# Optimization experiments

Hardware: AMD Instinct MI355X
Metric: run time of the kernel (lower is better)

Reference implementation:

```python
import jax, jax.numpy as jnp
import numpy as np

BN_EPS = 1e-5

def _bn(x, p):
    # p rows: gamma, beta, running_mean, running_var (eval-mode BatchNorm1d)
    g, b, m, v = p[0], p[1], p[2], p[3]
    return (x - m) * jax.lax.rsqrt(v + BN_EPS) * g + b

def setup_inputs() -> dict:
    key = jax.random.key(0)
    ks = iter(jax.random.split(key, 32))
    B, P, T, E, H = 16, 64, 8, 64, 64
    batch = B * P
    def w(shape, scale=0.1):
        return (jax.random.normal(next(ks), shape, dtype=jnp.float32) * scale)
    def bn_pack(d):
        k1, k2, k3, k4 = jax.random.split(next(ks), 4)
        gamma = 1.0 + 0.1 * jax.random.normal(k1, (d,), dtype=jnp.float32)
        beta = 0.1 * jax.random.normal(k2, (d,), dtype=jnp.float32)
        mean = 0.1 * jax.random.normal(k3, (d,), dtype=jnp.float32)
        var = 0.5 + jax.random.uniform(k4, (d,), dtype=jnp.float32)
        return jnp.stack([gamma, beta, mean, var], axis=0)
    return {
        "h_states": w((1, batch, H), 1.0),
        "end_pos": w((batch, 2), 1.0),
        "vx": w((T, batch), 1.0),
        "vy": w((T, batch), 1.0),
        "agent_type": jax.random.uniform(next(ks), (T, batch, 1), dtype=jnp.float32),
        "ws_w": w((2, E)), "ws_b": w((E,)),
        "wv_w": w((2, E)), "wv_b": w((E,)),
        "wa_w": w((6, E)), "wa_b": w((E,)),
        "att1_w": w((E, 1024)), "att1_b": w((1024,)), "att_bn1": bn_pack(1024),
        "att2_w": w((1024, 1)), "att2_b": w((1,)), "att_bn2": bn_pack(1),
        "pre1_w": w((E + H, 512)), "pre1_b": w((512,)), "pre_bn1": bn_pack(512),
        "pre2_w": w((512, 1024)), "pre2_b": w((1024,)), "pre_bn2": bn_pack(1024),
        "num_ped": P,
    }

def reference(h_states, end_pos, vx, vy, agent_type,
              ws_w, ws_b, wv_w, wv_b, wa_w, wa_b,
              att1_w, att1_b, att_bn1, att2_w, att2_b, att_bn2,
              pre1_w, pre1_b, pre_bn1, pre2_w, pre2_b, pre_bn2,
              num_ped):
    P = num_ped
    batch = end_pos.shape[0]
    B = batch // P  # uniform groups (seq_start_end = [(b*P, (b+1)*P)])
    H = h_states.shape[-1]
    h = h_states.reshape(batch, H).reshape(B, P, H)            # curr_hidden per group
    pos = end_pos.reshape(B, P, 2)
    # k = i*P + j: repeated row = pos[j], 'transposed' row = pos[i]
    rel = pos[:, None, :, :] - pos[:, :, None, :]               # [B, i, j, 2]
    rel_emb = rel @ ws_w + ws_b                                 # [B, i, j, E]
    # attention_mlp: Linear->BN->ReLU->Linear->BN->ReLU (make_mlp applies BN+act after every layer)
    a1 = jax.nn.relu(_bn(rel_emb @ att1_w + att1_b, att_bn1))   # [B, i, j, 1024]
    scores = jax.nn.relu(_bn(a1 @ att2_w + att2_b, att_bn2))    # [B, i, j, 1]
    # torch.softmax(scores, dim=1) on shape (n*n, 1): softmax over a singleton -> all ones
    aw = jax.nn.softmax(scores, axis=-1)
    # velocity embedding: computed in the original then discarded (dead code, kept for fidelity)
    vel = jnp.stack([vx[-1].reshape(B, P), vy[-1].reshape(B, P)], axis=-1)
    _vel_emb = vel @ wv_w + wv_b  # noqa: F841 (unused, matches original)
    # curr_agent_type.repeat(num_ped, 6): row k=i*P+j -> type[j] tiled to 6 features
    at6 = jnp.repeat(agent_type[0].reshape(B, P, 1), 6, axis=-1)  # [B, j, 6]
    at_emb = at6 @ wa_w + wa_b                                    # [B, j, E]
    feat_j = jnp.concatenate([h, at_emb], axis=-1)                # [B, j, H+E]
    weighted = jnp.broadcast_to(feat_j[:, None, :, :], (B, P, P, feat_j.shape[-1])) * (0.05 * aw)
    p1 = jax.nn.relu(_bn(weighted @ pre1_w + pre1_b, pre_bn1))    # [B, i, j, 512]
    p2 = jax.nn.relu(_bn(p1 @ pre2_w + pre2_b, pre_bn2))          # [B, i, j, 1024]
    pool = p2.max(axis=2)                                         # view(n,n,-1).max(1): max over j
    return pool.reshape(batch, -1)
```

## Files before the change

### kernel.cpp

```cpp
#include <hip/hip_runtime.h>
#include <hip/hip_bf16.h>

#define BN_EPS 1e-5f

typedef float f32x4 __attribute__((ext_vector_type(4)));
typedef __bf16 bfx8 __attribute__((ext_vector_type(8)));


__global__ __launch_bounds__(256) void k0_prep(
    const float* __restrict__ w2, const float* __restrict__ w1,
    __bf16* __restrict__ w2t, __bf16* __restrict__ w1t)
{
    __shared__ float tile[64][69];
    const int t = threadIdx.x;
    int kt0, n0, src_ld, dst_ld;
    const float* src;
    __bf16* dst;
    if (blockIdx.x < 128) {
        kt0 = (blockIdx.x & 7) * 64;  n0 = (blockIdx.x >> 3) * 64;
        src = w2; src_ld = 1024; dst = w2t; dst_ld = 512;
    } else {
        const int bt = blockIdx.x - 128;
        kt0 = (bt & 1) * 64;  n0 = (bt >> 1) * 64;
        src = w1; src_ld = 512; dst = w1t; dst_ld = 128;
    }
    #pragma unroll
    for (int i = 0; i < 4; ++i) {
        const int idx = t + i * 256;
        const int kk  = idx >> 4;
        const int nq  = (idx & 15) * 4;
        const f32x4 val = *(const f32x4*)&src[(size_t)(kt0 + kk) * src_ld + n0 + nq];
        #pragma unroll
        for (int j = 0; j < 4; ++j) tile[kk][nq + j] = val[j];
    }
    __syncthreads();
    #pragma unroll
    for (int i = 0; i < 2; ++i) {
        const int idx = t + i * 256;
        const int n   = idx >> 3;
        const int kq  = (idx & 7) * 8;
        bfx8 o;
        #pragma unroll
        for (int j = 0; j < 8; ++j) o[j] = (__bf16)tile[kq + j][n];
        *(bfx8*)&dst[(size_t)(n0 + n) * dst_ld + kt0 + kq] = o;
    }
}

__global__ __launch_bounds__(512, 2) void kmain(
    const float* __restrict__ h,
    const float* __restrict__ at,
    const float* __restrict__ wa_w,
    const float* __restrict__ wa_b,
    const __bf16* __restrict__ w1t,
    const float* __restrict__ b1,
    const float* __restrict__ bn1,
    const __bf16* __restrict__ w2t,
    const float* __restrict__ b2,
    const float* __restrict__ bn2,
    float* __restrict__ out)
{
    const int cc   = blockIdx.x;
    const int b    = blockIdx.y;
    const int t    = threadIdx.x;
    const int wid  = t >> 6;
    const int lane = t & 63;
    const int l15  = lane & 15;
    const int lhi  = lane >> 4;

    __shared__ __bf16 x_lds[64][136];
    __shared__ __bf16 p1_lds[64][520];
    __shared__ __bf16 B2_lds[64][520];
    __shared__ float  red[4][64];

    f32x4 b2stage[8];
    {
        const char* base = (const char*)w2t + (size_t)(cc * 64) * 1024;
        #pragma unroll
        for (int i = 0; i < 8; ++i) {
            const int n = i * 8 + wid;
            b2stage[i] = *(const f32x4*)(base + (size_t)n * 1024 + lane * 16);
        }
    }

    if (t < 64) {
        float s = 0.f;
        #pragma unroll
        for (int q = 0; q < 6; ++q) s += wa_w[q * 64 + t];
        red[0][t] = s;
    }
    __syncthreads();

    #pragma unroll
    for (int i = 0; i < 2; ++i) {
        const int idx = t + i * 512;
        const int rr  = idx >> 4;
        const int cg  = (idx & 15) * 8;
        bfx8 o;
        if (cg < 64) {
            const f32x4 v0 = *(const f32x4*)&h[(size_t)(b * 64 + rr) * 64 + cg];
            const f32x4 v1 = *(const f32x4*)&h[(size_t)(b * 64 + rr) * 64 + cg + 4];
            #pragma unroll
            for (int j = 0; j < 4; ++j) {
                o[j]     = (__bf16)(0.05f * v0[j]);
                o[4 + j] = (__bf16)(0.05f * v1[j]);
            }
        } else {
            const float a = at[b * 64 + rr];
            #pragma unroll
            for (int j = 0; j < 8; ++j) {
                const int e = cg - 64 + j;
                o[j] = (__bf16)(0.05f * fmaf(a, red[0][e], wa_b[e]));
            }
        }
        *(bfx8*)&x_lds[rr][cg] = o;
    }
    __syncthreads();

    const int n0w = wid * 64;
    bfx8 b1r[16];
    #pragma unroll
    for (int ks = 0; ks < 4; ++ks)
        #pragma unroll
        for (int nf = 0; nf < 4; ++nf)
            b1r[ks * 4 + nf] = *(const bfx8*)(w1t +
                (size_t)(n0w + nf * 16 + l15) * 128 + ks * 32 + lhi * 8);

    f32x4 acc1[4][4] = {};
    #pragma unroll
    for (int ks = 0; ks < 4; ++ks) {
        bfx8 a[4];
        #pragma unroll
        for (int mf = 0; mf < 4; ++mf)
            a[mf] = *(const bfx8*)&x_lds[mf * 16 + l15][ks * 32 + lhi * 8];
        #pragma unroll
        for (int mf = 0; mf < 4; ++mf)
            #pragma unroll
            for (int nf = 0; nf < 4; ++nf)
                acc1[mf][nf] = __builtin_amdgcn_mfma_f32_16x16x32_bf16(
                    a[mf], b1r[ks * 4 + nf], acc1[mf][nf], 0, 0, 0);
    }

    #pragma unroll
    for (int nf = 0; nf < 4; ++nf) {
        const int c    = n0w + nf * 16 + l15;
        const float s  = rsqrtf(bn1[1536 + c] + BN_EPS) * bn1[c];
        const float be = bn1[512 + c];
        const float mu = bn1[1024 + c];
        const float bias = b1[c];
        #pragma unroll
        for (int mf = 0; mf < 4; ++mf)
            #pragma unroll
            for (int r = 0; r < 4; ++r) {
                const float val =
                    fmaxf((acc1[mf][nf][r] + bias - mu) * s + be, 0.f);
                p1_lds[mf * 16 + lhi * 4 + r][c] = (__bf16)val;
            }
    }

    #pragma unroll
    for (int i = 0; i < 8; ++i) {
        const int n = i * 8 + wid;
        *(f32x4*)((char*)&B2_lds[0][0] + (size_t)n * 1040 + lane * 16) =
            b2stage[i];
    }
    __syncthreads();

    const int mw = wid >> 1;
    const int nw = wid & 1;
    f32x4 acc2[2] = {};
    #pragma unroll
    for (int ks = 0; ks < 16; ++ks) {
        const bfx8 a = *(const bfx8*)&p1_lds[mw * 16 + l15][ks * 32 + lhi * 8];
        #pragma unroll
        for (int f = 0; f < 2; ++f) {
            const bfx8 bb =
                *(const bfx8*)&B2_lds[nw * 32 + f * 16 + l15][ks * 32 + lhi * 8];
            acc2[f] = __builtin_amdgcn_mfma_f32_16x16x32_bf16(a, bb, acc2[f], 0, 0, 0);
        }
    }

    #pragma unroll
    for (int f = 0; f < 2; ++f) {
        const int cg   = cc * 64 + nw * 32 + f * 16 + l15;
        const float s  = rsqrtf(bn2[3072 + cg] + BN_EPS) * bn2[cg];
        const float be = bn2[1024 + cg];
        const float mu = bn2[2048 + cg];
        const float bias = b2[cg];
        float mm = 0.f;
        #pragma unroll
        for (int r = 0; r < 4; ++r) {
            const float val = (acc2[f][r] + bias - mu) * s + be;
            mm = fmaxf(mm, fmaxf(val, 0.f));
        }
        mm = fmaxf(mm, __shfl_xor(mm, 16));
        mm = fmaxf(mm, __shfl_xor(mm, 32));
        if (lane < 16) red[mw][nw * 32 + f * 16 + lane] = mm;
    }
    __syncthreads();

    const int cl   = t & 63;
    const int iseg = t >> 6;
    const float pool = fmaxf(fmaxf(red[0][cl], red[1][cl]),
                             fmaxf(red[2][cl], red[3][cl]));
    const int ob = (b * 64 + iseg * 8) * 1024 + cc * 64 + cl;
    #pragma unroll
    for (int ii = 0; ii < 8; ++ii) out[ob + ii * 1024] = pool;
}

extern "C" void kernel_launch(void* const* d_in, const int* in_sizes, int n_in,
                              void* d_out, int out_size, void* d_ws, size_t ws_size,
                              hipStream_t stream) {
    const float* h    = (const float*)d_in[0];
    const float* at   = (const float*)d_in[4];
    const float* wa_w = (const float*)d_in[9];
    const float* wa_b = (const float*)d_in[10];
    const float* w1   = (const float*)d_in[17];
    const float* b1   = (const float*)d_in[18];
    const float* bn1  = (const float*)d_in[19];
    const float* w2   = (const float*)d_in[20];
    const float* b2   = (const float*)d_in[21];
    const float* bn2  = (const float*)d_in[22];

    char* ws = (char*)d_ws;
    __bf16* w2t = (__bf16*)ws;
    __bf16* w1t = (__bf16*)(ws + (1 << 20));
    float*  out = (float*)d_out;

    k0_prep<<<144, 256, 0, stream>>>(w2, w1, w2t, w1t);
    kmain<<<dim3(16, 16), 512, 0, stream>>>(h, at, wa_w, wa_b,
                                            w1t, b1, bn1, w2t, b2, bn2, out);
}
```

Baseline: 21.06 us.

## Hoist activation prep and BN folding into prep kernel; vectorize LDS and output stores

```diff
diff --git a/kernel.cpp b/kernel.cpp
--- a/kernel.cpp
+++ b/kernel.cpp
@@ -5,58 +5,107 @@
 
 typedef float f32x4 __attribute__((ext_vector_type(4)));
 typedef __bf16 bfx8 __attribute__((ext_vector_type(8)));
+typedef __bf16 bfx4 __attribute__((ext_vector_type(4)));
 
 
 __global__ __launch_bounds__(256) void k0_prep(
     const float* __restrict__ w2, const float* __restrict__ w1,
-    __bf16* __restrict__ w2t, __bf16* __restrict__ w1t)
+    const float* __restrict__ h, const float* __restrict__ at,
+    const float* __restrict__ wa_w, const float* __restrict__ wa_b,
+    const float* __restrict__ b1, const float* __restrict__ bn1,
+    const float* __restrict__ b2, const float* __restrict__ bn2,
+    __bf16* __restrict__ w2t, __bf16* __restrict__ w1t,
+    __bf16* __restrict__ xg, float* __restrict__ scsh)
 {
-    __shared__ float tile[64][69];
-    const int t = threadIdx.x;
-    int kt0, n0, src_ld, dst_ld;
-    const float* src;
-    __bf16* dst;
-    if (blockIdx.x < 128) {
-        kt0 = (blockIdx.x & 7) * 64;  n0 = (blockIdx.x >> 3) * 64;
-        src = w2; src_ld = 1024; dst = w2t; dst_ld = 512;
+    const int t  = threadIdx.x;
+    const int bx = blockIdx.x;
+
+    if (bx < 144) {
+        __shared__ float tile[64][69];
+        int kt0, n0, src_ld, dst_ld;
+        const float* src;
+        __bf16* dst;
+        if (bx < 128) {
+            kt0 = (bx & 7) * 64;  n0 = (bx >> 3) * 64;
+            src = w2; src_ld = 1024; dst = w2t; dst_ld = 512;
+        } else {
+            const int bt = bx - 128;
+            kt0 = (bt & 1) * 64;  n0 = (bt >> 1) * 64;
+            src = w1; src_ld = 512; dst = w1t; dst_ld = 128;
+        }
+        #pragma unroll
+        for (int i = 0; i < 4; ++i) {
+            const int idx = t + i * 256;
+            const int kk  = idx >> 4;
+            const int nq  = (idx & 15) * 4;
+            const f32x4 val = *(const f32x4*)&src[(size_t)(kt0 + kk) * src_ld + n0 + nq];
+            #pragma unroll
+            for (int j = 0; j < 4; ++j) tile[kk][nq + j] = val[j];
+        }
+        __syncthreads();
+        #pragma unroll
+        for (int i = 0; i < 2; ++i) {
+            const int idx = t + i * 256;
+            const int n   = idx >> 3;
+            const int kq  = (idx & 7) * 8;
+            bfx8 o;
+            #pragma unroll
+            for (int j = 0; j < 8; ++j) o[j] = (__bf16)tile[kq + j][n];
+            *(bfx8*)&dst[(size_t)(n0 + n) * dst_ld + kt0 + kq] = o;
+        }
+    } else if (bx < 160) {
+        __shared__ float S[64];
+        const int r0 = (bx - 144) * 64;
+        if (t < 64) {
+            float s = 0.f;
+            #pragma unroll
+            for (int q = 0; q < 6; ++q) s += wa_w[q * 64 + t];
+            S[t] = s;
+        }
+        __syncthreads();
+        #pragma unroll
+        for (int i = 0; i < 4; ++i) {
+            const int idx = t + i * 256;
+            const int row = idx >> 4;
+            const int cg  = (idx & 15) * 8;
+            bfx8 o;
+            if (cg < 64) {
+                const f32x4 v0 = *(const f32x4*)&h[(size_t)(r0 + row) * 64 + cg];
+                const f32x4 v1 = *(const f32x4*)&h[(size_t)(r0 + row) * 64 + cg + 4];
+                #pragma unroll
+                for (int j = 0; j < 4; ++j) {
+                    o[j]     = (__bf16)(0.05f * v0[j]);
+                    o[4 + j] = (__bf16)(0.05f * v1[j]);
+                }
+            } else {
+                const float a = at[r0 + row];
+                #pragma unroll
+                for (int j = 0; j < 8; ++j) {
+                    const int e = cg - 64 + j;
+                    o[j] = (__bf16)(0.05f * fmaf(a, S[e], wa_b[e]));
+                }
+            }
+            *(bfx8*)&xg[(size_t)(r0 + row) * 128 + cg] = o;
+        }
     } else {
-        const int bt = blockIdx.x - 128;
-        kt0 = (bt & 1) * 64;  n0 = (bt >> 1) * 64;
-        src = w1; src_ld = 512; dst = w1t; dst_ld = 128;
-    }
-    #pragma unroll
-    for (int i = 0; i < 4; ++i) {
-        const int idx = t + i * 256;
-        const int kk  = idx >> 4;
-        const int nq  = (idx & 15) * 4;
-        const f32x4 val = *(const f32x4*)&src[(size_t)(kt0 + kk) * src_ld + n0 + nq];
-        #pragma unroll
-        for (int j = 0; j < 4; ++j) tile[kk][nq + j] = val[j];
-    }
-    __syncthreads();
-    #pragma unroll
-    for (int i = 0; i < 2; ++i) {
-        const int idx = t + i * 256;
-        const int n   = idx >> 3;
-        const int kq  = (idx & 7) * 8;
-        bfx8 o;
-        #pragma unroll
-        for (int j = 0; j < 8; ++j) o[j] = (__bf16)tile[kq + j][n];
-        *(bfx8*)&dst[(size_t)(n0 + n) * dst_ld + kt0 + kq] = o;
+        for (int c = t; c < 512; c += 256) {
+            const float s = rsqrtf(bn1[1536 + c] + BN_EPS) * bn1[c];
+            scsh[c]       = s;
+            scsh[512 + c] = (b1[c] - bn1[1024 + c]) * s + bn1[512 + c];
+        }
+        for (int c = t; c < 1024; c += 256) {
+            const float s  = rsqrtf(bn2[3072 + c] + BN_EPS) * bn2[c];
+            scsh[1024 + c] = s;
+            scsh[2048 + c] = (b2[c] - bn2[2048 + c]) * s + bn2[1024 + c];
+        }
     }
 }
 
 __global__ __launch_bounds__(512, 2) void kmain(
-    const float* __restrict__ h,
-    const float* __restrict__ at,
-    const float* __restrict__ wa_w,
-    const float* __restrict__ wa_b,
+    const __bf16* __restrict__ xg,
     const __bf16* __restrict__ w1t,
-    const float* __restrict__ b1,
-    const float* __restrict__ bn1,
     const __bf16* __restrict__ w2t,
-    const float* __restrict__ b2,
-    const float* __restrict__ bn2,
+    const float* __restrict__ scsh,
     float* __restrict__ out)
 {
     const int cc   = blockIdx.x;
@@ -74,86 +123,63 @@
 
     f32x4 b2stage[8];
     {
-        const char* base = (const char*)w2t + (size_t)(cc * 64) * 1024;
+        const __bf16* base = w2t + (size_t)(cc * 64) * 512;
         #pragma unroll
         for (int i = 0; i < 8; ++i) {
             const int n = i * 8 + wid;
-            b2stage[i] = *(const f32x4*)(base + (size_t)n * 1024 + lane * 16);
-        }
-    }
-
-    if (t < 64) {
-        float s = 0.f;
-        #pragma unroll
-        for (int q = 0; q < 6; ++q) s += wa_w[q * 64 + t];
-        red[0][t] = s;
-    }
-    __syncthreads();
+            b2stage[i] = *(const f32x4*)(base + (size_t)n * 512 + lane * 8);
+        }
+    }
 
     #pragma unroll
     for (int i = 0; i < 2; ++i) {
         const int idx = t + i * 512;
-        const int rr  = idx >> 4;
+        const int row = idx >> 4;
         const int cg  = (idx & 15) * 8;
-        bfx8 o;
-        if (cg < 64) {
-            const f32x4 v0 = *(const f32x4*)&h[(size_t)(b * 64 + rr) * 64 + cg];
-            const f32x4 v1 = *(const f32x4*)&h[(size_t)(b * 64 + rr) * 64 + cg + 4];
-            #pragma unroll
-            for (int j = 0; j < 4; ++j) {
-                o[j]     = (__bf16)(0.05f * v0[j]);
-                o[4 + j] = (__bf16)(0.05f * v1[j]);
-            }
-        } else {
-            const float a = at[b * 64 + rr];
-            #pragma unroll
-            for (int j = 0; j < 8; ++j) {
-                const int e = cg - 64 + j;
-                o[j] = (__bf16)(0.05f * fmaf(a, red[0][e], wa_b[e]));
-            }
-        }
-        *(bfx8*)&x_lds[rr][cg] = o;
+        *(bfx8*)&x_lds[row][cg] =
+            *(const bfx8*)&xg[(size_t)(b * 64 + row) * 128 + cg];
     }
     __syncthreads();
 
-    const int n0w = wid * 64;
-    bfx8 b1r[16];
-    #pragma unroll
-    for (int ks = 0; ks < 4; ++ks)
-        #pragma unroll
-        for (int nf = 0; nf < 4; ++nf)
-            b1r[ks * 4 + nf] = *(const bfx8*)(w1t +
-                (size_t)(n0w + nf * 16 + l15) * 128 + ks * 32 + lhi * 8);
-
+    const int c0w = wid * 64;
     f32x4 acc1[4][4] = {};
     #pragma unroll
     for (int ks = 0; ks < 4; ++ks) {
-        bfx8 a[4];
+        bfx8 af[4];
+        #pragma unroll
+        for (int cf = 0; cf < 4; ++cf)
+            af[cf] = *(const bfx8*)&w1t[(size_t)(c0w + cf * 16 + l15) * 128 +
+                                        ks * 32 + lhi * 8];
+        bfx8 bf_[4];
         #pragma unroll
         for (int mf = 0; mf < 4; ++mf)
-            a[mf] = *(const bfx8*)&x_lds[mf * 16 + l15][ks * 32 + lhi * 8];
-        #pragma unroll
-        for (int mf = 0; mf < 4; ++mf)
-            #pragma unroll
-            for (int nf = 0; nf < 4; ++nf)
-                acc1[mf][nf] = __builtin_amdgcn_mfma_f32_16x16x32_bf16(
-                    a[mf], b1r[ks * 4 + nf], acc1[mf][nf], 0, 0, 0);
-    }
-
-    #pragma unroll
-    for (int nf = 0; nf < 4; ++nf) {
-        const int c    = n0w + nf * 16 + l15;
-        const float s  = rsqrtf(bn1[1536 + c] + BN_EPS) * bn1[c];
-        const float be = bn1[512 + c];
-        const float mu = bn1[1024 + c];
-        const float bias = b1[c];
-        #pragma unroll
-        for (int mf = 0; mf < 4; ++mf)
-            #pragma unroll
-            for (int r = 0; r < 4; ++r) {
-                const float val =
-                    fmaxf((acc1[mf][nf][r] + bias - mu) * s + be, 0.f);
-                p1_lds[mf * 16 + lhi * 4 + r][c] = (__bf16)val;
+            bf_[mf] = *(const bfx8*)&x_lds[mf * 16 + l15][ks * 32 + lhi * 8];
+        #pragma unroll
+        for (int cf = 0; cf < 4; ++cf)
+            #pragma unroll
+            for (int mf = 0; mf < 4; ++mf)
+                acc1[cf][mf] = __builtin_amdgcn_mfma_f32_16x16x32_bf16(
+                    af[cf], bf_[mf], acc1[cf][mf], 0, 0, 0);
+    }
+
+    {
+        f32x4 sc[4], sh[4];
+        #pragma unroll
+        for (int cf = 0; cf < 4; ++cf) {
+            const int c4 = c0w + cf * 16 + lhi * 4;
+            sc[cf] = *(const f32x4*)&scsh[c4];
+            sh[cf] = *(const f32x4*)&scsh[512 + c4];
+        }
+        #pragma unroll
+        for (int cf = 0; cf < 4; ++cf)
+            #pragma unroll
+            for (int mf = 0; mf < 4; ++mf) {
+                bfx4 pk;
+                #pragma unroll
+                for (int r = 0; r < 4; ++r)
+                    pk[r] = (__bf16)fmaxf(
+                        fmaf(acc1[cf][mf][r], sc[cf][r], sh[cf][r]), 0.f);
+                *(bfx4*)&p1_lds[mf * 16 + l15][c0w + cf * 16 + lhi * 4] = pk;
             }
     }
 
@@ -165,46 +191,50 @@
     }
     __syncthreads();
 
-    const int mw = wid >> 1;
-    const int nw = wid & 1;
+    const int mrow  = (wid >> 1) * 16;
+    const int nbase = (wid & 1) * 32;
     f32x4 acc2[2] = {};
     #pragma unroll
     for (int ks = 0; ks < 16; ++ks) {
-        const bfx8 a = *(const bfx8*)&p1_lds[mw * 16 + l15][ks * 32 + lhi * 8];
-        #pragma unroll
-        for (int f = 0; f < 2; ++f) {
+        const bfx8 a = *(const bfx8*)&p1_lds[mrow + l15][ks * 32 + lhi * 8];
+        #pragma unroll
+        for (int nf = 0; nf < 2; ++nf) {
             const bfx8 bb =
-                *(const bfx8*)&B2_lds[nw * 32 + f * 16 + l15][ks * 32 + lhi * 8];
-            acc2[f] = __builtin_amdgcn_mfma_f32_16x16x32_bf16(a, bb, acc2[f], 0, 0, 0);
-        }
-    }
-
-    #pragma unroll
-    for (int f = 0; f < 2; ++f) {
-        const int cg   = cc * 64 + nw * 32 + f * 16 + l15;
-        const float s  = rsqrtf(bn2[3072 + cg] + BN_EPS) * bn2[cg];
-        const float be = bn2[1024 + cg];
-        const float mu = bn2[2048 + cg];
-        const float bias = b2[cg];
+                *(const bfx8*)&B2_lds[nbase + nf * 16 + l15][ks * 32 + lhi * 8];
+            acc2[nf] = __builtin_amdgcn_mfma_f32_16x16x32_bf16(a, bb, acc2[nf], 0, 0, 0);
+        }
+    }
+
+    #pragma unroll
+    for (int nf = 0; nf < 2; ++nf) {
+        const int ng  = cc * 64 + nbase + nf * 16 + l15;
+        const float s2 = scsh[1024 + ng];
+        const float h2 = scsh[2048 + ng];
         float mm = 0.f;
         #pragma unroll
-        for (int r = 0; r < 4; ++r) {
-            const float val = (acc2[f][r] + bias - mu) * s + be;
-            mm = fmaxf(mm, fmaxf(val, 0.f));
-        }
+        for (int r = 0; r < 4; ++r)
+            mm = fmaxf(mm, fmaxf(fmaf(acc2[nf][r], s2, h2), 0.f));
         mm = fmaxf(mm, __shfl_xor(mm, 16));
         mm = fmaxf(mm, __shfl_xor(mm, 32));
-        if (lane < 16) red[mw][nw * 32 + f * 16 + lane] = mm;
+        if (lane < 16) red[wid >> 1][nbase + nf * 16 + lane] = mm;
     }
     __syncthreads();
 
-    const int cl   = t & 63;
-    const int iseg = t >> 6;
-    const float pool = fmaxf(fmaxf(red[0][cl], red[1][cl]),
-                             fmaxf(red[2][cl], red[3][cl]));
-    const int ob = (b * 64 + iseg * 8) * 1024 + cc * 64 + cl;
-    #pragma unroll
-    for (int ii = 0; ii < 8; ++ii) out[ob + ii * 1024] = pool;
+    #pragma unroll
+    for (int i = 0; i < 2; ++i) {
+        const int q   = t + i * 512;
+        const int row = q >> 4;
+        const int cq  = (q & 15) * 4;
+        const f32x4 r0 = *(const f32x4*)&red[0][cq];
+        const f32x4 r1 = *(const f32x4*)&red[1][cq];
+        const f32x4 r2 = *(const f32x4*)&red[2][cq];
+        const f32x4 r3 = *(const f32x4*)&red[3][cq];
+        f32x4 pv;
+        #pragma unroll
+        for (int j = 0; j < 4; ++j)
+            pv[j] = fmaxf(fmaxf(r0[j], r1[j]), fmaxf(r2[j], r3[j]));
+        *(f32x4*)&out[(size_t)(b * 64 + row) * 1024 + cc * 64 + cq] = pv;
+    }
 }
 
 extern "C" void kernel_launch(void* const* d_in, const int* in_sizes, int n_in,
@@ -224,9 +254,11 @@
     char* ws = (char*)d_ws;
     __bf16* w2t = (__bf16*)ws;
     __bf16* w1t = (__bf16*)(ws + (1 << 20));
-    float*  out = (float*)d_out;
-
-    k0_prep<<<144, 256, 0, stream>>>(w2, w1, w2t, w1t);
-    kmain<<<dim3(16, 16), 512, 0, stream>>>(h, at, wa_w, wa_b,
-                                            w1t, b1, bn1, w2t, b2, bn2, out);
+    __bf16* xg  = (__bf16*)(ws + (1 << 20) + (128 << 10));
+    float*  scsh = (float*)(ws + (1 << 20) + (384 << 10));
+    float*  out  = (float*)d_out;
+
+    k0_prep<<<161, 256, 0, stream>>>(w2, w1, h, at, wa_w, wa_b,
+                                     b1, bn1, b2, bn2, w2t, w1t, xg, scsh);
+    kmain<<<dim3(16, 16), 512, 0, stream>>>(xg, w1t, w2t, scsh, out);
 }
```

New measurement: 19.64 us. -6.7%, faster.
